# Kernel tuning notes

Measured on AMD Instinct MI355X. Metric: run time of the kernel, lower is better.

Reference implementation:

```python
import jax, jax.numpy as jnp
import numpy as np

TEMPERATURE = 0.07
NORM_EPS = 1e-12   # F.normalize eps
LOG_EPS = 1e-08


def setup_inputs() -> dict:
    key = jax.random.key(0)
    k1, k2 = jax.random.split(key)
    N, D, C = 8192, 512, 64
    projections = jax.random.normal(k1, (N, D), dtype=jnp.float32)
    targets = jax.random.randint(k2, (N,), 0, C, dtype=jnp.int64)
    return {"projections": projections, "targets": targets}


def reference(projections, targets):
    # L2-normalize rows (matches F.normalize: x / max(||x||, eps))
    norm = jnp.linalg.norm(projections, axis=1, keepdims=True)
    p = projections / jnp.maximum(norm, NORM_EPS)

    # [N, N] cosine similarity / temperature
    sim = jnp.matmul(p, p.T) / TEMPERATURE
    # row-max subtraction for numerical stability (gradient flows through max,
    # as in the torch original)
    sim = sim - jnp.max(sim, axis=1, keepdims=True)
    exp_sim = jnp.exp(sim)

    n = projections.shape[0]
    eye = jnp.eye(n, dtype=bool)
    mask_self = ~eye                                   # exclude self-pairs
    mask_pos = (targets[:, None] == targets[None, :]) & mask_self

    denom = jnp.sum(jnp.where(mask_self, exp_sim, 0.0), axis=1, keepdims=True)
    log_prob = sim - jnp.log(denom + LOG_EPS)

    num = jnp.sum(jnp.where(mask_pos, log_prob, 0.0), axis=1)
    cnt = jnp.sum(mask_pos, axis=1).astype(log_prob.dtype)
    # divide_no_nan: 0 where cnt == 0
    loss_per_sample = jnp.where(cnt == 0, 0.0, num / jnp.where(cnt == 0, 1.0, cnt))
    return loss_per_sample
```

## Files before the change

kernel.cpp:

```cpp
#include <hip/hip_runtime.h>
#include <hip/hip_bf16.h>
#include <math.h>

#define N_ROWS 8192
#define DIM    512
#define NCLS   64
#define BM     128
#define BK     64
#define NTILE  (N_ROWS / BM)
#define NTRI   (NTILE * (NTILE + 1) / 2)
#define M_CONST 14.285714285714286f
#define SCALE_SQRT 3.7796447300922722f

using bf16x8 = __attribute__((ext_vector_type(8))) short;
using f32x4  = __attribute__((ext_vector_type(4))) float;

static __device__ inline unsigned short f2bf(float x) {
  unsigned u = __float_as_uint(x);
  unsigned r = u + 0x7FFFu + ((u >> 16) & 1u);
  return (unsigned short)(r >> 16);
}

__global__ __launch_bounds__(256) void normalize_rows(const float* __restrict__ proj,
                                                      unsigned short* __restrict__ outb) {
  const int row  = blockIdx.x * 4 + (threadIdx.x >> 6);
  const int lane = threadIdx.x & 63;
  const float4* src = (const float4*)(proj + (size_t)row * DIM);
  float4 a = src[lane * 2];
  float4 b = src[lane * 2 + 1];
  float ss = a.x*a.x + a.y*a.y + a.z*a.z + a.w*a.w
           + b.x*b.x + b.y*b.y + b.z*b.z + b.w*b.w;
#pragma unroll
  for (int off = 1; off < 64; off <<= 1) ss += __shfl_xor(ss, off);
  const float scale = SCALE_SQRT / fmaxf(sqrtf(ss), 1e-12f);
  float v[8] = {a.x, a.y, a.z, a.w, b.x, b.y, b.z, b.w};
  unsigned short h[8];
#pragma unroll
  for (int i = 0; i < 8; ++i) h[i] = f2bf(v[i] * scale);
  uint4 packed;
  packed.x = (unsigned)h[0] | ((unsigned)h[1] << 16);
  packed.y = (unsigned)h[2] | ((unsigned)h[3] << 16);
  packed.z = (unsigned)h[4] | ((unsigned)h[5] << 16);
  packed.w = (unsigned)h[6] | ((unsigned)h[7] << 16);
  *(uint4*)(outb + (size_t)row * DIM + lane * 8) = packed;
}

__global__ __launch_bounds__(1024) void class_hist(const int* __restrict__ tgt,
                                                   int* __restrict__ hist) {
  __shared__ int h[16][NCLS];
  const int wid = threadIdx.x >> 6;
  const int lane = threadIdx.x & 63;
  if (lane < NCLS) h[wid][lane] = 0;
  __syncthreads();
  for (int i = threadIdx.x; i < N_ROWS; i += 1024) atomicAdd(&h[wid][tgt[i]], 1);
  __syncthreads();
  if (threadIdx.x < NCLS) {
    int s = 0;
#pragma unroll
    for (int w = 0; w < 16; ++w) s += h[w][threadIdx.x];
    hist[threadIdx.x] = s;
  }
}

__global__ __launch_bounds__(256, 2) void supcon_tile(const unsigned short* __restrict__ p16,
                                                      const int* __restrict__ tgt,
                                                      float* __restrict__ dpart,
                                                      float* __restrict__ spart) {
  int rem = blockIdx.x, br = 0;
  while (rem >= NTILE - br) { rem -= NTILE - br; ++br; }
  const int bc = br + rem;

  __shared__ short As[2][BM * BK];
  __shared__ short Bs[2][BM * BK];
  __shared__ int tgr[BM], tgc[BM];

  const int tid  = threadIdx.x;
  const int lane = tid & 63;
  const int wid  = tid >> 6;
  const int wr = wid >> 1, wc = wid & 1;
  const int lhi = lane >> 4, llo = lane & 15;
  const int lsw = llo & 7;

  const int r_ld = tid >> 3;
  const int gp   = tid & 7;
  const size_t rowA0 = (size_t)br * BM;
  const size_t rowB0 = (size_t)bc * BM;

#define STAGE(BUF, KT) do {                                                          \
  _Pragma("unroll")                                                                  \
  for (int c = 0; c < 4; ++c) {                                                      \
    const int r  = c * 32 + r_ld;                                                    \
    const int gl = gp ^ (r & 7);                    \
    const unsigned short* gA = p16 + (rowA0 + r) * DIM + (KT) * BK + gl * 8;         \
    const unsigned short* gB = p16 + (rowB0 + r) * DIM + (KT) * BK + gl * 8;         \
    __builtin_amdgcn_global_load_lds((const __attribute__((address_space(1))) void*)gA, \
        (__attribute__((address_space(3))) void*)&As[BUF][r * BK + gp * 8], 16, 0, 0);  \
    __builtin_amdgcn_global_load_lds((const __attribute__((address_space(1))) void*)gB, \
        (__attribute__((address_space(3))) void*)&Bs[BUF][r * BK + gp * 8], 16, 0, 0);  \
  }                                                                                  \
} while (0)

  STAGE(0, 0);
  if (tid < BM)            tgr[tid] = tgt[br * BM + tid];
  else if (tid < 2 * BM)   tgc[tid - BM] = tgt[bc * BM + (tid - BM)];

  f32x4 zero = {0.f, 0.f, 0.f, 0.f};
  f32x4 acc[4][4];
#pragma unroll
  for (int i = 0; i < 4; ++i)
#pragma unroll
    for (int j = 0; j < 4; ++j) acc[i][j] = zero;

  __syncthreads();

  int cur = 0;
  for (int kt = 0; kt < DIM / BK; ++kt) {
    if (kt + 1 < DIM / BK) STAGE(cur ^ 1, kt + 1);
#pragma unroll
    for (int ks = 0; ks < 2; ++ks) {
      bf16x8 af[4], bfr[4];
#pragma unroll
      for (int mi = 0; mi < 4; ++mi) {
        const int Ra = wr * 64 + mi * 16 + llo;
        af[mi] = *(const bf16x8*)&As[cur][Ra * BK + (((ks * 4 + lhi) ^ lsw) * 8)];
      }
#pragma unroll
      for (int ni = 0; ni < 4; ++ni) {
        const int Rb = wc * 64 + ni * 16 + llo;
        bfr[ni] = *(const bf16x8*)&Bs[cur][Rb * BK + (((ks * 4 + lhi) ^ lsw) * 8)];
      }
#pragma unroll
      for (int mi = 0; mi < 4; ++mi)
#pragma unroll
        for (int ni = 0; ni < 4; ++ni)
          acc[mi][ni] = __builtin_amdgcn_mfma_f32_16x16x32_bf16(af[mi], bfr[ni], acc[mi][ni], 0, 0, 0);
    }
    __syncthreads();
    cur ^= 1;
  }
#undef STAGE

  const bool diag = (br == bc);
  float ecol[4] = {0.f, 0.f, 0.f, 0.f};
  float scol[4] = {0.f, 0.f, 0.f, 0.f};

#pragma unroll
  for (int mi = 0; mi < 4; ++mi) {
#pragma unroll
    for (int rg = 0; rg < 4; ++rg) {
      const int rin  = wr * 64 + mi * 16 + lhi * 4 + rg;
      const int trow = tgr[rin];
      float esum = 0.f, ssum = 0.f;
#pragma unroll
      for (int ni = 0; ni < 4; ++ni) {
        const int cin = wc * 64 + ni * 16 + llo;
        const float sim = acc[mi][ni][rg];
        const bool self = diag && (rin == cin);
        const float e = self ? 0.f : __expf(sim - M_CONST);
        const bool pos = (!self) && (trow == tgc[cin]);
        const float sv = pos ? sim : 0.f;
        esum += e;  ssum += sv;
        ecol[ni] += e;  scol[ni] += sv;
      }
#pragma unroll
      for (int off = 1; off < 16; off <<= 1) {
        esum += __shfl_xor(esum, off);
        ssum += __shfl_xor(ssum, off);
      }
      if (llo == 0) {
        const int grow = br * BM + rin;
        dpart[(size_t)(bc * 2 + wc) * N_ROWS + grow] = esum;
        spart[(size_t)(bc * 2 + wc) * N_ROWS + grow] = ssum;
      }
    }
  }

  if (!diag) {
#pragma unroll
    for (int ni = 0; ni < 4; ++ni) {
      float ec = ecol[ni], sc = scol[ni];
      ec += __shfl_xor(ec, 16); ec += __shfl_xor(ec, 32);
      sc += __shfl_xor(sc, 16); sc += __shfl_xor(sc, 32);
      if (lhi == 0) {
        const int gcol = bc * BM + wc * 64 + ni * 16 + llo;
        dpart[(size_t)(br * 2 + wr) * N_ROWS + gcol] = ec;
        spart[(size_t)(br * 2 + wr) * N_ROWS + gcol] = sc;
      }
    }
  }
}

__global__ __launch_bounds__(256) void combine_loss(const float* __restrict__ dpart,
                                                    const float* __restrict__ spart,
                                                    const int* __restrict__ tgt,
                                                    const int* __restrict__ hist,
                                                    float* __restrict__ out) {
  __shared__ float dsh[4][64], ssh[4][64];
  const int lane = threadIdx.x & 63;
  const int g    = threadIdx.x >> 6;
  const int r    = blockIdx.x * 64 + lane;
  float d = 0.f, s = 0.f;
  for (int k = g * 32; k < g * 32 + 32; ++k) {
    d += dpart[(size_t)k * N_ROWS + r];
    s += spart[(size_t)k * N_ROWS + r];
  }
  dsh[g][lane] = d; ssh[g][lane] = s;
  __syncthreads();
  if (g == 0) {
    d = dsh[0][lane] + dsh[1][lane] + dsh[2][lane] + dsh[3][lane];
    s = ssh[0][lane] + ssh[1][lane] + ssh[2][lane] + ssh[3][lane];
    const int cnt = hist[tgt[r]] - 1;
    out[r] = (cnt > 0) ? (s / (float)cnt - M_CONST - logf(d + 1e-8f)) : 0.f;
  }
}

extern "C" void kernel_launch(void* const* d_in, const int* in_sizes, int n_in,
                              void* d_out, int out_size, void* d_ws, size_t ws_size,
                              hipStream_t stream) {
  const float* proj = (const float*)d_in[0];
  const int*   tgt  = (const int*)d_in[1];
  float* out = (float*)d_out;

  char* ws = (char*)d_ws;
  unsigned short* p16  = (unsigned short*)ws;
  float* dpart = (float*)(ws + (size_t)8  * 1024 * 1024);
  float* spart = (float*)(ws + (size_t)12 * 1024 * 1024);
  int*   hist  = (int*)(ws + (size_t)16 * 1024 * 1024);

  normalize_rows<<<N_ROWS / 4, 256, 0, stream>>>(proj, p16);
  class_hist<<<1, 1024, 0, stream>>>(tgt, hist);
  supcon_tile<<<NTRI, 256, 0, stream>>>(p16, tgt, dpart, spart);
  combine_loss<<<N_ROWS / 64, 256, 0, stream>>>(dpart, spart, tgt, hist, out);
}
```

Measured before the change: 91.87 us.

## Enlarge symmetric Gram tiles to 256 with 8 waves and interleaved prefetch

Doubles the tile to 256x256 with 512-thread blocks (8 waves, each computing 128x64), so global/LDS traffic per MFMA drops and the triangular tile count falls from 2080 to 528. The next K-slice prefetch is split into four parts interleaved between MFMA phases, with barriers and s_setprio. Per-block row and column partials are reduced in LDS before a single store, which shrinks the partial buffers and the combine pass. Blocks are remapped in strides of 8 across the triangle. This costs more LDS (about 132 KB) and registers, and the smaller grid (528 blocks) may leave compute units underfilled on the tail.

```diff
diff --git a/kernel.cpp b/kernel.cpp
--- a/kernel.cpp
+++ b/kernel.cpp
@@ -5,8 +5,9 @@
 #define N_ROWS 8192
 #define DIM    512
 #define NCLS   64
-#define BM     128
+#define BM     256
 #define BK     64
+#define NKT    (DIM / BK)
 #define NTILE  (N_ROWS / BM)
 #define NTRI   (NTILE * (NTILE + 1) / 2)
 #define M_CONST 14.285714285714286f
@@ -62,98 +63,119 @@
   }
 }
 
-__global__ __launch_bounds__(256, 2) void supcon_tile(const unsigned short* __restrict__ p16,
+__global__ __launch_bounds__(512, 2) void supcon_tile(const unsigned short* __restrict__ p16,
                                                       const int* __restrict__ tgt,
                                                       float* __restrict__ dpart,
                                                       float* __restrict__ spart) {
-  int rem = blockIdx.x, br = 0;
+  const int logical = ((int)blockIdx.x & 7) * (NTRI / 8) + ((int)blockIdx.x >> 3);
+  int rem = logical, br = 0;
   while (rem >= NTILE - br) { rem -= NTILE - br; ++br; }
   const int bc = br + rem;
 
   __shared__ short As[2][BM * BK];
   __shared__ short Bs[2][BM * BK];
-  __shared__ int tgr[BM], tgc[BM];
+  __shared__ int   tgr[BM], tgc[BM];
+  __shared__ float redE[4][BM], redS[4][BM];
+  __shared__ float redEc[2][BM], redSc[2][BM];
 
   const int tid  = threadIdx.x;
   const int lane = tid & 63;
   const int wid  = tid >> 6;
-  const int wr = wid >> 1, wc = wid & 1;
+  const int wm = wid >> 2, wn = wid & 3;
   const int lhi = lane >> 4, llo = lane & 15;
-  const int lsw = llo & 7;
-
-  const int r_ld = tid >> 3;
-  const int gp   = tid & 7;
+
   const size_t rowA0 = (size_t)br * BM;
   const size_t rowB0 = (size_t)bc * BM;
 
-#define STAGE(BUF, KT) do {                                                          \
-  _Pragma("unroll")                                                                  \
-  for (int c = 0; c < 4; ++c) {                                                      \
-    const int r  = c * 32 + r_ld;                                                    \
-    const int gl = gp ^ (r & 7);                    \
-    const unsigned short* gA = p16 + (rowA0 + r) * DIM + (KT) * BK + gl * 8;         \
-    const unsigned short* gB = p16 + (rowB0 + r) * DIM + (KT) * BK + gl * 8;         \
-    __builtin_amdgcn_global_load_lds((const __attribute__((address_space(1))) void*)gA, \
-        (__attribute__((address_space(3))) void*)&As[BUF][r * BK + gp * 8], 16, 0, 0);  \
-    __builtin_amdgcn_global_load_lds((const __attribute__((address_space(1))) void*)gB, \
-        (__attribute__((address_space(3))) void*)&Bs[BUF][r * BK + gp * 8], 16, 0, 0);  \
-  }                                                                                  \
+#define STAGE_HALF(XS, BUF, ROW0, H, KT) do {                                   \
+  _Pragma("unroll")                                                             \
+  for (int j = 0; j < 2; ++j) {                                                 \
+    const int g  = wid * 64 + lane + j * 512;                                   \
+    const int r  = (H) * 128 + (g >> 3);                                        \
+    const int gl = (g & 7) ^ (r & 7);                                           \
+    const unsigned short* src = p16 + ((ROW0) + r) * DIM + (KT) * BK + gl * 8;  \
+    __builtin_amdgcn_global_load_lds(                                           \
+        (const __attribute__((address_space(1))) void*)src,                     \
+        (__attribute__((address_space(3))) void*)&XS[BUF][(H) * 8192 + g * 8],  \
+        16, 0, 0);                                                              \
+  }                                                                             \
 } while (0)
 
-  STAGE(0, 0);
-  if (tid < BM)            tgr[tid] = tgt[br * BM + tid];
-  else if (tid < 2 * BM)   tgc[tid - BM] = tgt[bc * BM + (tid - BM)];
+  STAGE_HALF(As, 0, rowA0, 0, 0);
+  STAGE_HALF(As, 0, rowA0, 1, 0);
+  STAGE_HALF(Bs, 0, rowB0, 0, 0);
+  STAGE_HALF(Bs, 0, rowB0, 1, 0);
+  if (tid < BM) tgr[tid] = tgt[br * BM + tid];
+  else          tgc[tid - BM] = tgt[bc * BM + (tid - BM)];
 
   f32x4 zero = {0.f, 0.f, 0.f, 0.f};
-  f32x4 acc[4][4];
-#pragma unroll
-  for (int i = 0; i < 4; ++i)
+  f32x4 acc[8][4];
+#pragma unroll
+  for (int i = 0; i < 8; ++i)
 #pragma unroll
     for (int j = 0; j < 4; ++j) acc[i][j] = zero;
 
   __syncthreads();
 
   int cur = 0;
-  for (int kt = 0; kt < DIM / BK; ++kt) {
-    if (kt + 1 < DIM / BK) STAGE(cur ^ 1, kt + 1);
-#pragma unroll
-    for (int ks = 0; ks < 2; ++ks) {
-      bf16x8 af[4], bfr[4];
+  for (int kt = 0; kt < NKT; ++kt) {
+    const int nxt = cur ^ 1;
+    const bool pf = (kt + 1 < NKT);
+
+    bf16x8 bfr[4][2];
+#pragma unroll
+    for (int ni = 0; ni < 4; ++ni)
+#pragma unroll
+      for (int ks = 0; ks < 2; ++ks) {
+        const int Rb = wn * 64 + ni * 16 + llo;
+        bfr[ni][ks] = *(const bf16x8*)&Bs[cur][Rb * BK + (((ks * 4 + lhi) ^ (Rb & 7)) * 8)];
+      }
+
+#pragma unroll
+    for (int ph = 0; ph < 4; ++ph) {
+      const int h = ph >> 1, ks = ph & 1;
+      bf16x8 af[4];
 #pragma unroll
       for (int mi = 0; mi < 4; ++mi) {
-        const int Ra = wr * 64 + mi * 16 + llo;
-        af[mi] = *(const bf16x8*)&As[cur][Ra * BK + (((ks * 4 + lhi) ^ lsw) * 8)];
-      }
-#pragma unroll
-      for (int ni = 0; ni < 4; ++ni) {
-        const int Rb = wc * 64 + ni * 16 + llo;
-        bfr[ni] = *(const bf16x8*)&Bs[cur][Rb * BK + (((ks * 4 + lhi) ^ lsw) * 8)];
-      }
+        const int Ra = wm * 128 + h * 64 + mi * 16 + llo;
+        af[mi] = *(const bf16x8*)&As[cur][Ra * BK + (((ks * 4 + lhi) ^ (Ra & 7)) * 8)];
+      }
+      if (pf) {
+        if (ph == 0)      STAGE_HALF(As, nxt, rowA0, 0, kt + 1);
+        else if (ph == 1) STAGE_HALF(As, nxt, rowA0, 1, kt + 1);
+        else if (ph == 2) STAGE_HALF(Bs, nxt, rowB0, 0, kt + 1);
+        else              STAGE_HALF(Bs, nxt, rowB0, 1, kt + 1);
+      }
+      __builtin_amdgcn_s_barrier();
+      __builtin_amdgcn_s_setprio(1);
 #pragma unroll
       for (int mi = 0; mi < 4; ++mi)
 #pragma unroll
         for (int ni = 0; ni < 4; ++ni)
-          acc[mi][ni] = __builtin_amdgcn_mfma_f32_16x16x32_bf16(af[mi], bfr[ni], acc[mi][ni], 0, 0, 0);
+          acc[h * 4 + mi][ni] =
+              __builtin_amdgcn_mfma_f32_16x16x32_bf16(af[mi], bfr[ni][ks], acc[h * 4 + mi][ni], 0, 0, 0);
+      __builtin_amdgcn_s_setprio(0);
+      if (ph < 3) __builtin_amdgcn_s_barrier();
     }
     __syncthreads();
-    cur ^= 1;
-  }
-#undef STAGE
+    cur = nxt;
+  }
+#undef STAGE_HALF
 
   const bool diag = (br == bc);
   float ecol[4] = {0.f, 0.f, 0.f, 0.f};
   float scol[4] = {0.f, 0.f, 0.f, 0.f};
 
 #pragma unroll
-  for (int mi = 0; mi < 4; ++mi) {
+  for (int mi = 0; mi < 8; ++mi) {
 #pragma unroll
     for (int rg = 0; rg < 4; ++rg) {
-      const int rin  = wr * 64 + mi * 16 + lhi * 4 + rg;
+      const int rin  = wm * 128 + mi * 16 + lhi * 4 + rg;
       const int trow = tgr[rin];
       float esum = 0.f, ssum = 0.f;
 #pragma unroll
       for (int ni = 0; ni < 4; ++ni) {
-        const int cin = wc * 64 + ni * 16 + llo;
+        const int cin = wn * 64 + ni * 16 + llo;
         const float sim = acc[mi][ni][rg];
         const bool self = diag && (rin == cin);
         const float e = self ? 0.f : __expf(sim - M_CONST);
@@ -167,14 +189,9 @@
         esum += __shfl_xor(esum, off);
         ssum += __shfl_xor(ssum, off);
       }
-      if (llo == 0) {
-        const int grow = br * BM + rin;
-        dpart[(size_t)(bc * 2 + wc) * N_ROWS + grow] = esum;
-        spart[(size_t)(bc * 2 + wc) * N_ROWS + grow] = ssum;
-      }
+      if (llo == 0) { redE[wn][rin] = esum; redS[wn][rin] = ssum; }
     }
   }
-
   if (!diag) {
 #pragma unroll
     for (int ni = 0; ni < 4; ++ni) {
@@ -182,11 +199,22 @@
       ec += __shfl_xor(ec, 16); ec += __shfl_xor(ec, 32);
       sc += __shfl_xor(sc, 16); sc += __shfl_xor(sc, 32);
       if (lhi == 0) {
-        const int gcol = bc * BM + wc * 64 + ni * 16 + llo;
-        dpart[(size_t)(br * 2 + wr) * N_ROWS + gcol] = ec;
-        spart[(size_t)(br * 2 + wr) * N_ROWS + gcol] = sc;
+        redEc[wm][wn * 64 + ni * 16 + llo] = ec;
+        redSc[wm][wn * 64 + ni * 16 + llo] = sc;
       }
     }
+  }
+  __syncthreads();
+
+  if (tid < BM) {
+    const float e = redE[0][tid] + redE[1][tid] + redE[2][tid] + redE[3][tid];
+    const float s = redS[0][tid] + redS[1][tid] + redS[2][tid] + redS[3][tid];
+    dpart[(size_t)bc * N_ROWS + rowA0 + tid] = e;
+    spart[(size_t)bc * N_ROWS + rowA0 + tid] = s;
+  } else if (!diag) {
+    const int c = tid - BM;
+    dpart[(size_t)br * N_ROWS + rowB0 + c] = redEc[0][c] + redEc[1][c];
+    spart[(size_t)br * N_ROWS + rowB0 + c] = redSc[0][c] + redSc[1][c];
   }
 }
 
@@ -200,7 +228,7 @@
   const int g    = threadIdx.x >> 6;
   const int r    = blockIdx.x * 64 + lane;
   float d = 0.f, s = 0.f;
-  for (int k = g * 32; k < g * 32 + 32; ++k) {
+  for (int k = g * 8; k < g * 8 + 8; ++k) {
     d += dpart[(size_t)k * N_ROWS + r];
     s += spart[(size_t)k * N_ROWS + r];
   }
@@ -223,12 +251,12 @@
 
   char* ws = (char*)d_ws;
   unsigned short* p16  = (unsigned short*)ws;
-  float* dpart = (float*)(ws + (size_t)8  * 1024 * 1024);
-  float* spart = (float*)(ws + (size_t)12 * 1024 * 1024);
-  int*   hist  = (int*)(ws + (size_t)16 * 1024 * 1024);
+  float* dpart = (float*)(ws + (size_t)8 * 1024 * 1024);
+  float* spart = (float*)(ws + (size_t)9 * 1024 * 1024);
+  int*   hist  = (int*)(ws + (size_t)10 * 1024 * 1024);
 
   normalize_rows<<<N_ROWS / 4, 256, 0, stream>>>(proj, p16);
   class_hist<<<1, 1024, 0, stream>>>(tgt, hist);
-  supcon_tile<<<NTRI, 256, 0, stream>>>(p16, tgt, dpart, spart);
+  supcon_tile<<<NTRI, 512, 0, stream>>>(p16, tgt, dpart, spart);
   combine_loss<<<N_ROWS / 64, 256, 0, stream>>>(dpart, spart, tgt, hist, out);
 }
```

After: 101.4 us. 1.1x slower.
